# Kernel optimization log

Measured on AMD Instinct MI355X. Metric: run time of the kernel, lower is better.

## Reference

```python
import jax, jax.numpy as jnp
import numpy as np

G, N, E, F, C, H = 2, 20000, 160000, 128, 64, 8
NEG_SLOPE = 0.2


def setup_inputs() -> dict:
    key = jax.random.key(0)
    ks = jax.random.split(key, 16)
    def w(k, shape, fan_in):
        return jax.random.normal(k, shape, jnp.float32) * (1.0 / np.sqrt(fan_in))
    z = lambda *s: jnp.zeros(s, jnp.float32)
    return {
        "x": jax.random.normal(ks[0], (G, N, F), jnp.float32),
        "edge_index": jax.random.randint(ks[1], (G, 2, E), 0, N, jnp.int32),
        "edge_weight": jax.random.uniform(ks[2], (G, E), jnp.float32),
        "Wl1": w(ks[3], (F, H * C), F), "bl1": z(H * C),
        "Wr1": w(ks[4], (F, H * C), F), "br1": z(H * C),
        "We1": w(ks[5], (1, H * C), 1),
        "att1": w(ks[6], (H, C), C),
        "bias1": z(H * C),
        "Wl2": w(ks[7], (H * C, C), H * C), "bl2": z(C),
        "Wr2": w(ks[8], (H * C, C), H * C), "br2": z(C),
        "We2": w(ks[9], (1, C), 1),
        "att2": w(ks[10], (1, C), C),
        "bias2": z(C),
        "Wg": w(ks[11], (C, C), C), "bg": z(C),
        "Wn": w(ks[12], (2 * C, C), 2 * C), "bn": z(C),
        "Wo": w(ks[13], (C, 1), C), "bo": z(1),
    }


def _segment_softmax(logits, seg, n):
    m = jax.ops.segment_max(logits, seg, num_segments=n)
    ex = jnp.exp(logits - m[seg])
    den = jax.ops.segment_sum(ex, seg, num_segments=n)
    return ex / den[seg]


def _gatv2(x, src, dst, eattr, Wl, bl, Wr, br, We, att, bias, heads, concat):
    # Faithful PyG GATv2Conv (share_weights=False, edge_dim=1).
    n = x.shape[0]
    hc = Wl.shape[1]
    c = hc // heads
    xl = (x @ Wl + bl).reshape(n, heads, c)   # lin_l (source / message)
    xr = (x @ Wr + br).reshape(n, heads, c)   # lin_r (target)
    ee = (eattr @ We).reshape(-1, heads, c)   # lin_edge (bias=False)
    s = jax.nn.leaky_relu(xl[src] + xr[dst] + ee, NEG_SLOPE)  # [Etot, H, C]
    logit = jnp.einsum('ehc,hc->eh', s, att)
    alpha = _segment_softmax(logit, dst, n)   # softmax over incoming edges
    out = jax.ops.segment_sum(alpha[..., None] * xl[src], dst, num_segments=n)
    out = out.reshape(n, hc) if concat else out.mean(axis=1)
    return out + bias


def _forward(edge_index, x, edge_weight, Wl1, bl1, Wr1, br1, We1, att1, bias1,
             Wl2, bl2, Wr2, br2, We2, att2, bias2, Wg, bg, Wn, bn, Wo, bo):
    n = x.shape[1]
    def per_graph(xg, eig, ewg):
        src, dst = eig[0], eig[1]
        ea = ewg[:, None]  # edge_weight.unsqueeze(-1), edge_dim=1
        # add_self_loops with fill_value='mean' (mean of edge_attr grouped by dst)
        cnt = jax.ops.segment_sum(jnp.ones_like(ewg), dst, num_segments=n)
        loop = jax.ops.segment_sum(ea, dst, num_segments=n) / jnp.clip(cnt, 1.0)[:, None]
        ar = jnp.arange(n, dtype=src.dtype)
        src2 = jnp.concatenate([src, ar])
        dst2 = jnp.concatenate([dst, ar])
        ea2 = jnp.concatenate([ea, loop], axis=0)
        h = jax.nn.elu(_gatv2(xg, src2, dst2, ea2, Wl1, bl1, Wr1, br1, We1, att1, bias1, H, True))
        h = jax.nn.elu(_gatv2(h, src2, dst2, ea2, Wl2, bl2, Wr2, br2, We2, att2, bias2, 1, False))
        return h
    h = jax.vmap(per_graph)(x, edge_index, edge_weight)      # [G, N, C]
    g_emb = h.max(axis=1)                                    # global_max_pool per graph
    Gv = g_emb.max(axis=0)                                   # max over graphs -> [C]
    Gv = jax.nn.relu(Gv @ Wg + bg)
    Hc = jnp.concatenate([h, jnp.broadcast_to(Gv, h.shape)], axis=-1)  # [G,N,2C]
    h2 = jax.nn.relu(Hc @ Wn + bn)
    return (h2 @ Wo + bo)[..., 0]                            # [G, N] logits


def reference(x, edge_index, edge_weight, Wl1, bl1, Wr1, br1, We1, att1, bias1,
              Wl2, bl2, Wr2, br2, We2, att2, bias2, Wg, bg, Wn, bn, Wo, bo):
    return _forward(edge_index, x, edge_weight, Wl1, bl1, Wr1, br1, We1, att1, bias1,
                    Wl2, bl2, Wr2, br2, We2, att2, bias2, Wg, bg, Wn, bn, Wo, bo)
```

## Files before the change

kernel.cpp:

```cpp
#include <hip/hip_runtime.h>
#include <hip/hip_bf16.h>
#include <cstdint>
#include <cstddef>

#define NEG_SLOPE 0.2f

static constexpr int Gg = 2;
static constexpr int Nn = 20000;
static constexpr int Ee = 160000;
static constexpr int Ff = 128;
static constexpr int Cc = 64;
static constexpr int HC = 512;
static constexpr int GN = Gg * Nn;
static constexpr int GNP = 40064;
static constexpr int DEGMAX = 48;

typedef __attribute__((ext_vector_type(8))) short short8;
typedef __attribute__((ext_vector_type(4))) float floatx4;

__device__ __forceinline__ float bf2f(unsigned short b) {
    return __uint_as_float(((unsigned)b) << 16);
}
__device__ __forceinline__ unsigned short f2bf(float x) {
    unsigned u = __float_as_uint(x);
    unsigned r = 0x7fffu + ((u >> 16) & 1u);
    return (unsigned short)((u + r) >> 16);
}
__device__ __forceinline__ void unpack8(const uint4 p, float* f) {
    f[0] = __uint_as_float(p.x << 16); f[1] = __uint_as_float(p.x & 0xffff0000u);
    f[2] = __uint_as_float(p.y << 16); f[3] = __uint_as_float(p.y & 0xffff0000u);
    f[4] = __uint_as_float(p.z << 16); f[5] = __uint_as_float(p.z & 0xffff0000u);
    f[6] = __uint_as_float(p.w << 16); f[7] = __uint_as_float(p.w & 0xffff0000u);
}
__device__ __forceinline__ void unpack4(const uint2 p, float* f) {
    f[0] = __uint_as_float(p.x << 16); f[1] = __uint_as_float(p.x & 0xffff0000u);
    f[2] = __uint_as_float(p.y << 16); f[3] = __uint_as_float(p.y & 0xffff0000u);
}
__device__ __forceinline__ unsigned encf(float x) {
    unsigned u = __float_as_uint(x);
    return (u & 0x80000000u) ? ~u : (u | 0x80000000u);
}
__device__ __forceinline__ float decf(unsigned e) {
    return __uint_as_float((e & 0x80000000u) ? (e ^ 0x80000000u) : ~e);
}

__global__ void castprep_k(const float* __restrict__ x, unsigned short* __restrict__ xb,
                           const float* __restrict__ Wl1, const float* __restrict__ Wr1,
                           const float* __restrict__ bl1, const float* __restrict__ br1,
                           const float* __restrict__ Wl2, const float* __restrict__ Wr2,
                           const float* __restrict__ bl2, const float* __restrict__ br2,
                           unsigned short* __restrict__ Wt1, unsigned short* __restrict__ Wt2,
                           float* __restrict__ b1cat, float* __restrict__ b2cat,
                           int* __restrict__ cnt, unsigned* __restrict__ gmax) {
    int t = blockIdx.x * 256 + threadIdx.x;
    size_t base = (size_t)t * 4;
    if (base < (size_t)GNP * Ff) {
        ushort4 ov;
        if (base < (size_t)GN * Ff) {
            float4 v = *(const float4*)(x + base);
            ov.x = f2bf(v.x); ov.y = f2bf(v.y); ov.z = f2bf(v.z); ov.w = f2bf(v.w);
        } else {
            ov.x = ov.y = ov.z = ov.w = 0;
        }
        *(ushort4*)(xb + base) = ov;
    }
    if (t < 1024 * 128) {
        int n = t >> 7, k = t & 127;
        float v = (n < 512) ? Wl1[(size_t)k * 512 + n] : Wr1[(size_t)k * 512 + n - 512];
        Wt1[t] = f2bf(v);
    }
    if (t < 128 * 512) {
        int n = t >> 9, k = t & 511;
        float v = (n < 64) ? Wl2[(size_t)k * 64 + n] : Wr2[(size_t)k * 64 + n - 64];
        Wt2[t] = f2bf(v);
    }
    if (t < 1024) b1cat[t] = (t < 512) ? bl1[t] : br1[t - 512];
    if (t < 128)  b2cat[t] = (t < 64) ? bl2[t] : br2[t - 64];
    if (t < GN)   cnt[t] = 0;
    if (t < 1024) gmax[t] = 0u;
}

template <int K, bool EDGES>
__global__ __launch_bounds__(256) void mfma_gemm_k(const unsigned short* __restrict__ A, int lda,
                                                   const unsigned short* __restrict__ Bt,
                                                   const float* __restrict__ bias,
                                                   unsigned short* __restrict__ Cg, int ldc,
                                                   int Mreal,
                                                   const int* __restrict__ ei,
                                                   const float* __restrict__ ew,
                                                   int* __restrict__ cnt,
                                                   int2* __restrict__ sedge) {
    if (EDGES) {
        int bid = blockIdx.y * gridDim.x + blockIdx.x;
        int idx = bid * 256 + threadIdx.x;
        if (idx < Gg * Ee) {
            int g = (idx >= Ee) ? 1 : 0;
            int e = idx - g * Ee;
            int src = ei[(size_t)g * 2 * Ee + e];
            int dst = ei[(size_t)g * 2 * Ee + Ee + e];
            float wv = ew[idx];
            int node = g * Nn + dst;
            int pos = atomicAdd(&cnt[node], 1);
            if (pos < DEGMAX) {
                int2 v; v.x = src; v.y = __float_as_int(wv);
                sedge[(size_t)node * DEGMAX + pos] = v;
            }
        }
    }

    __shared__ unsigned short As[128 * 32];
    __shared__ unsigned short Bs[128 * 32];
    const int t = threadIdx.x;
    const int lane = t & 63;
    const int wid = t >> 6;
    const int wm = wid >> 1, wn = wid & 1;
    const int m0 = blockIdx.x * 128;
    const int n0 = blockIdx.y * 128;

    floatx4 acc[4][4] = {};

    const int jrow = t >> 2;
    const int js = t & 3;
    const int wavebase = (t & 192) * 16;

    for (int k0 = 0; k0 < K; k0 += 32) {
#pragma unroll
        for (int r = 0; r < 2; ++r) {
            int row = jrow + r * 64;
            int c = js ^ ((row >> 1) & 3);
            const unsigned short* gA = A + (size_t)(m0 + row) * lda + k0 + c * 8;
            const unsigned short* gB = Bt + (size_t)(n0 + row) * K + k0 + c * 8;
            __builtin_amdgcn_global_load_lds(
                (const __attribute__((address_space(1))) void*)gA,
                (__attribute__((address_space(3))) void*)((char*)As + r * 4096 + wavebase),
                16, 0, 0);
            __builtin_amdgcn_global_load_lds(
                (const __attribute__((address_space(1))) void*)gB,
                (__attribute__((address_space(3))) void*)((char*)Bs + r * 4096 + wavebase),
                16, 0, 0);
        }
        __syncthreads();

        const int lrow = lane & 15, lc = lane >> 4;
        short8 af[4], bf[4];
#pragma unroll
        for (int i2 = 0; i2 < 4; ++i2) {
            int rA = wm * 64 + i2 * 16 + lrow;
            int sA = lc ^ ((rA >> 1) & 3);
            af[i2] = *(const short8*)((const char*)As + (rA * 4 + sA) * 16);
        }
#pragma unroll
        for (int j2 = 0; j2 < 4; ++j2) {
            int rB = wn * 64 + j2 * 16 + lrow;
            int sB = lc ^ ((rB >> 1) & 3);
            bf[j2] = *(const short8*)((const char*)Bs + (rB * 4 + sB) * 16);
        }
#pragma unroll
        for (int i2 = 0; i2 < 4; ++i2)
#pragma unroll
            for (int j2 = 0; j2 < 4; ++j2)
                acc[i2][j2] = __builtin_amdgcn_mfma_f32_16x16x32_bf16(bf[j2], af[i2], acc[i2][j2], 0, 0, 0);
        __syncthreads();
    }

    const int mrow = m0 + wm * 64 + (lane & 15);
    const int ncol0 = n0 + wn * 64 + ((lane >> 4) << 2);
    float4 bq[4];
#pragma unroll
    for (int j2 = 0; j2 < 4; ++j2) bq[j2] = *(const float4*)(bias + ncol0 + j2 * 16);
#pragma unroll
    for (int i2 = 0; i2 < 4; ++i2) {
        int m = mrow + i2 * 16;
        if (m < Mreal) {
#pragma unroll
            for (int j2 = 0; j2 < 4; ++j2) {
                ushort4 ov;
                ov.x = f2bf(acc[i2][j2][0] + bq[j2].x);
                ov.y = f2bf(acc[i2][j2][1] + bq[j2].y);
                ov.z = f2bf(acc[i2][j2][2] + bq[j2].z);
                ov.w = f2bf(acc[i2][j2][3] + bq[j2].w);
                *(ushort4*)(Cg + (size_t)m * ldc + ncol0 + j2 * 16) = ov;
            }
        }
    }
}

__global__ __launch_bounds__(256) void agg1_k(const unsigned short* xlr,
                                              const int2* __restrict__ sedge,
                                              const int* __restrict__ cnt,
                                              const float* __restrict__ att1, const float* __restrict__ We1,
                                              const float* __restrict__ bias1,
                                              unsigned short* h1, float* __restrict__ loopw) {
    const int lane = threadIdx.x & 63;
    const int node = (blockIdx.x << 2) + (threadIdx.x >> 6);
    if (node >= GN) return;
    const int g = (node >= Nn) ? 1 : 0;

    float attv[8], wev[8];
    {
        float4 a0 = *(const float4*)(att1 + lane * 8);
        float4 a1 = *(const float4*)(att1 + lane * 8 + 4);
        attv[0] = a0.x; attv[1] = a0.y; attv[2] = a0.z; attv[3] = a0.w;
        attv[4] = a1.x; attv[5] = a1.y; attv[6] = a1.z; attv[7] = a1.w;
        float4 w0 = *(const float4*)(We1 + lane * 8);
        float4 w1 = *(const float4*)(We1 + lane * 8 + 4);
        wev[0] = w0.x; wev[1] = w0.y; wev[2] = w0.z; wev[3] = w0.w;
        wev[4] = w1.x; wev[5] = w1.y; wev[6] = w1.z; wev[7] = w1.w;
    }
    float xrv[8];
    unpack8(((const uint4*)(xlr + (size_t)node * 1024 + 512))[lane], xrv);

    const int ec = cnt[node];
    const int2* ep = sedge + (size_t)node * DEGMAX;
    const uint4* rowb = (const uint4*)(xlr + (size_t)g * Nn * 1024) + lane;

    float lsum = 0.f, wsum = 0.f;
    float acc[8] = {};

    uint4 r0, r1; int2 s0v, s1v;
    if (ec > 0) { s0v = ep[0]; r0 = rowb[(size_t)s0v.x * 128]; }
    if (ec > 1) { s1v = ep[1]; r1 = rowb[(size_t)s1v.x * 128]; }
    int e = 0;
    while (e + 1 < ec) {
        uint4 r2, r3; int2 s2v, s3v;
        if (e + 2 < ec) { s2v = ep[e + 2]; r2 = rowb[(size_t)s2v.x * 128]; }
        if (e + 3 < ec) { s3v = ep[e + 3]; r3 = rowb[(size_t)s3v.x * 128]; }
        float xa[8], xb_[8];
        unpack8(r0, xa);
        unpack8(r1, xb_);
        float wa = __int_as_float(s0v.y), wb = __int_as_float(s1v.y);
        wsum += wa + wb;
        float ta = 0.f, tb = 0.f;
#pragma unroll
        for (int j = 0; j < 8; ++j) {
            float sa = xa[j] + fmaf(wa, wev[j], xrv[j]);
            float sb = xb_[j] + fmaf(wb, wev[j], xrv[j]);
            sa = fmaxf(sa, NEG_SLOPE * sa);
            sb = fmaxf(sb, NEG_SLOPE * sb);
            ta = fmaf(sa, attv[j], ta);
            tb = fmaf(sb, attv[j], tb);
        }
        ta += __shfl_xor(ta, 1); tb += __shfl_xor(tb, 1);
        ta += __shfl_xor(ta, 2); tb += __shfl_xor(tb, 2);
        ta += __shfl_xor(ta, 4); tb += __shfl_xor(tb, 4);
        float pa = __expf(ta), pb = __expf(tb);
        lsum += pa + pb;
#pragma unroll
        for (int j = 0; j < 8; ++j) acc[j] = fmaf(pa, xa[j], fmaf(pb, xb_[j], acc[j]));
        r0 = r2; s0v = s2v; r1 = r3; s1v = s3v;
        e += 2;
    }
    if (e < ec) {
        float xa[8];
        unpack8(r0, xa);
        float wa = __int_as_float(s0v.y);
        wsum += wa;
        float ta = 0.f;
#pragma unroll
        for (int j = 0; j < 8; ++j) {
            float sa = xa[j] + fmaf(wa, wev[j], xrv[j]);
            sa = fmaxf(sa, NEG_SLOPE * sa);
            ta = fmaf(sa, attv[j], ta);
        }
        ta += __shfl_xor(ta, 1); ta += __shfl_xor(ta, 2); ta += __shfl_xor(ta, 4);
        float pa = __expf(ta);
        lsum += pa;
#pragma unroll
        for (int j = 0; j < 8; ++j) acc[j] = fmaf(pa, xa[j], acc[j]);
    }

    float lw = wsum / fmaxf((float)ec, 1.f);
    {
        float xv[8];
        unpack8(((const uint4*)(xlr + (size_t)node * 1024))[lane], xv);
        float tp = 0.f;
#pragma unroll
        for (int j = 0; j < 8; ++j) {
            float s = xv[j] + fmaf(lw, wev[j], xrv[j]);
            s = fmaxf(s, NEG_SLOPE * s);
            tp = fmaf(s, attv[j], tp);
        }
        tp += __shfl_xor(tp, 1); tp += __shfl_xor(tp, 2); tp += __shfl_xor(tp, 4);
        float p = __expf(tp);
        lsum += p;
#pragma unroll
        for (int j = 0; j < 8; ++j) acc[j] = fmaf(p, xv[j], acc[j]);
    }

    float inv = 1.f / lsum;
    float4 b0 = *(const float4*)(bias1 + lane * 8);
    float4 b1 = *(const float4*)(bias1 + lane * 8 + 4);
    float bvv[8] = {b0.x, b0.y, b0.z, b0.w, b1.x, b1.y, b1.z, b1.w};
    float ov[8];
#pragma unroll
    for (int j = 0; j < 8; ++j) {
        float o = fmaf(acc[j], inv, bvv[j]);
        ov[j] = o > 0.f ? o : (__expf(o) - 1.f);
    }
    uint4 pk;
    pk.x = (unsigned)f2bf(ov[0]) | ((unsigned)f2bf(ov[1]) << 16);
    pk.y = (unsigned)f2bf(ov[2]) | ((unsigned)f2bf(ov[3]) << 16);
    pk.z = (unsigned)f2bf(ov[4]) | ((unsigned)f2bf(ov[5]) << 16);
    pk.w = (unsigned)f2bf(ov[6]) | ((unsigned)f2bf(ov[7]) << 16);
    ((uint4*)(h1 + (size_t)node * 1024))[lane] = pk;
    if (lane == 0) loopw[node] = lw;
}

__global__ __launch_bounds__(1024) void agg2_k(const unsigned short* __restrict__ xlr2,
                                               const int2* __restrict__ sedge,
                                               const int* __restrict__ cnt,
                                               const float* __restrict__ loopw,
                                               const float* __restrict__ att2, const float* __restrict__ We2,
                                               const float* __restrict__ bias2,
                                               float* __restrict__ hout, unsigned* __restrict__ gmax) {
    const int tid = threadIdx.x;
    const int lane = tid & 63;
    const int cs = lane & 15;
    const int sub = lane >> 4;
    const int node = blockIdx.x * 16 + (tid >> 6);
    const int g = (node >= Nn) ? 1 : 0;

    float4 av = *(const float4*)(att2 + cs * 4);
    float4 wv4 = *(const float4*)(We2 + cs * 4);
    float attv[4] = {av.x, av.y, av.z, av.w};
    float wevv[4] = {wv4.x, wv4.y, wv4.z, wv4.w};
    float xrv[4];
    unpack4(*(const uint2*)(xlr2 + (size_t)node * 128 + 64 + cs * 4), xrv);
    const unsigned short* rowb = xlr2 + (size_t)g * Nn * 128;

    const int ec = cnt[node];
    const int2* ep = sedge + (size_t)node * DEGMAX;
    const int lo = (ec * sub) >> 2;
    const int hi = (ec * (sub + 1)) >> 2;

    float lsum = 0.f, acc[4] = {};

    int e = lo;
    uint2 r0 = {0, 0}, r1 = {0, 0};
    int2 s0v = {0, 0}, s1v = {0, 0};
    if (e < hi)     { s0v = ep[e];     r0 = *(const uint2*)(rowb + (size_t)s0v.x * 128 + cs * 4); }
    if (e + 1 < hi) { s1v = ep[e + 1]; r1 = *(const uint2*)(rowb + (size_t)s1v.x * 128 + cs * 4); }
    while (e + 1 < hi) {
        uint2 r2 = {0, 0}, r3 = {0, 0};
        int2 s2v = {0, 0}, s3v = {0, 0};
        if (e + 2 < hi) { s2v = ep[e + 2]; r2 = *(const uint2*)(rowb + (size_t)s2v.x * 128 + cs * 4); }
        if (e + 3 < hi) { s3v = ep[e + 3]; r3 = *(const uint2*)(rowb + (size_t)s3v.x * 128 + cs * 4); }
        float xa[4], xb_[4];
        unpack4(r0, xa);
        unpack4(r1, xb_);
        float wa = __int_as_float(s0v.y), wb = __int_as_float(s1v.y);
        float ta = 0.f, tb = 0.f;
#pragma unroll
        for (int j = 0; j < 4; ++j) {
            float sa = xa[j] + fmaf(wa, wevv[j], xrv[j]);
            float sb = xb_[j] + fmaf(wb, wevv[j], xrv[j]);
            sa = fmaxf(sa, NEG_SLOPE * sa);
            sb = fmaxf(sb, NEG_SLOPE * sb);
            ta = fmaf(sa, attv[j], ta);
            tb = fmaf(sb, attv[j], tb);
        }
        ta += __shfl_xor(ta, 1); tb += __shfl_xor(tb, 1);
        ta += __shfl_xor(ta, 2); tb += __shfl_xor(tb, 2);
        ta += __shfl_xor(ta, 4); tb += __shfl_xor(tb, 4);
        ta += __shfl_xor(ta, 8); tb += __shfl_xor(tb, 8);
        float pa = __expf(ta), pb = __expf(tb);
        lsum += pa + pb;
#pragma unroll
        for (int j = 0; j < 4; ++j) acc[j] = fmaf(pa, xa[j], fmaf(pb, xb_[j], acc[j]));
        r0 = r2; s0v = s2v; r1 = r3; s1v = s3v;
        e += 2;
    }
    if (e < hi) {
        float xa[4];
        unpack4(r0, xa);
        float wa = __int_as_float(s0v.y);
        float ta = 0.f;
#pragma unroll
        for (int j = 0; j < 4; ++j) {
            float sa = xa[j] + fmaf(wa, wevv[j], xrv[j]);
            sa = fmaxf(sa, NEG_SLOPE * sa);
            ta = fmaf(sa, attv[j], ta);
        }
        ta += __shfl_xor(ta, 1); ta += __shfl_xor(ta, 2);
        ta += __shfl_xor(ta, 4); ta += __shfl_xor(ta, 8);
        float pa = __expf(ta);
        lsum += pa;
#pragma unroll
        for (int j = 0; j < 4; ++j) acc[j] = fmaf(pa, xa[j], acc[j]);
    }

    lsum += __shfl_xor(lsum, 16); lsum += __shfl_xor(lsum, 32);
#pragma unroll
    for (int j = 0; j < 4; ++j) {
        acc[j] += __shfl_xor(acc[j], 16);
        acc[j] += __shfl_xor(acc[j], 32);
    }

    {
        float lw = loopw[node];
        float xv[4];
        unpack4(*(const uint2*)(xlr2 + (size_t)node * 128 + cs * 4), xv);
        float tp = 0.f;
#pragma unroll
        for (int j = 0; j < 4; ++j) {
            float s = xv[j] + fmaf(lw, wevv[j], xrv[j]);
            s = fmaxf(s, NEG_SLOPE * s);
            tp = fmaf(s, attv[j], tp);
        }
        tp += __shfl_xor(tp, 1); tp += __shfl_xor(tp, 2);
        tp += __shfl_xor(tp, 4); tp += __shfl_xor(tp, 8);
        float p = __expf(tp);
        lsum += p;
#pragma unroll
        for (int j = 0; j < 4; ++j) acc[j] = fmaf(p, xv[j], acc[j]);
    }

    float inv = 1.f / lsum;
    float4 bv = *(const float4*)(bias2 + cs * 4);
    float bvv[4] = {bv.x, bv.y, bv.z, bv.w};
    float ov[4];
#pragma unroll
    for (int j = 0; j < 4; ++j) {
        float o = fmaf(acc[j], inv, bvv[j]);
        ov[j] = o > 0.f ? o : (__expf(o) - 1.f);
    }
    if (sub == 0) {
        float4 o4;
        o4.x = ov[0]; o4.y = ov[1]; o4.z = ov[2]; o4.w = ov[3];
        *(float4*)(hout + (size_t)node * Cc + cs * 4) = o4;
    }

    __shared__ unsigned bm[64];
    if (tid < 64) bm[tid] = 0u;
    __syncthreads();
    if (sub == 0) {
#pragma unroll
        for (int j = 0; j < 4; ++j) atomicMax(&bm[cs * 4 + j], encf(ov[j]));
    }
    __syncthreads();
    if (tid < 64) atomicMax(&gmax[tid * 16], bm[tid]);
}

__global__ __launch_bounds__(256) void final_k(const float* __restrict__ h,
                                               const unsigned* __restrict__ gmax,
                                               const float* __restrict__ Wg, const float* __restrict__ bg,
                                               const float* __restrict__ Wn, const float* __restrict__ bn,
                                               const float* __restrict__ Wo, const float* __restrict__ bo,
                                               float* __restrict__ out) {
    __shared__ float wns[64 * 64];
    __shared__ float g0s[64], g1s[64], cvs[64];
    const int tid = threadIdx.x;
    for (int k = tid; k < 64 * 64; k += 256) wns[k] = Wn[k];
    if (tid < 64) g0s[tid] = decf(gmax[tid * 16]);
    __syncthreads();
    if (tid < 64) {
        float a = bg[tid];
        for (int c = 0; c < 64; ++c) a += g0s[c] * Wg[c * 64 + tid];
        g1s[tid] = fmaxf(a, 0.f);
    }
    __syncthreads();
    if (tid < 64) {
        float b = bn[tid];
        for (int c = 0; c < 64; ++c) b += g1s[c] * Wn[(64 + c) * 64 + tid];
        cvs[tid] = b;
    }
    __syncthreads();

    const int lane = tid & 63;
    const int cs = lane & 15;
    const int sub = lane >> 4;
    const int node = blockIdx.x * 16 + (tid >> 6) * 4 + sub;

    float4 h4 = *(const float4*)(h + (size_t)node * Cc + cs * 4);
    float hv[4] = {h4.x, h4.y, h4.z, h4.w};
    float inner[4] = {cvs[cs * 4 + 0], cvs[cs * 4 + 1], cvs[cs * 4 + 2], cvs[cs * 4 + 3]};
#pragma unroll
    for (int c = 0; c < 64; ++c) {
        float hc = __shfl(hv[c & 3], sub * 16 + (c >> 2));
        float4 wv = *(const float4*)&wns[c * 64 + cs * 4];
        inner[0] = fmaf(hc, wv.x, inner[0]);
        inner[1] = fmaf(hc, wv.y, inner[1]);
        inner[2] = fmaf(hc, wv.z, inner[2]);
        inner[3] = fmaf(hc, wv.w, inner[3]);
    }
    float4 wo4 = *(const float4*)(Wo + cs * 4);
    float woa[4] = {wo4.x, wo4.y, wo4.z, wo4.w};
    float t = 0.f;
#pragma unroll
    for (int j = 0; j < 4; ++j) {
        float v = fmaxf(inner[j], 0.f);
        t = fmaf(v, woa[j], t);
    }
    t += __shfl_xor(t, 1); t += __shfl_xor(t, 2);
    t += __shfl_xor(t, 4); t += __shfl_xor(t, 8);
    if (cs == 0) out[node] = t + bo[0];
}

extern "C" void kernel_launch(void* const* d_in, const int* in_sizes, int n_in,
                              void* d_out, int out_size, void* d_ws, size_t ws_size,
                              hipStream_t stream) {
    const float* x     = (const float*)d_in[0];
    const int*   ei    = (const int*)d_in[1];
    const float* ew    = (const float*)d_in[2];
    const float* Wl1   = (const float*)d_in[3];
    const float* bl1v  = (const float*)d_in[4];
    const float* Wr1   = (const float*)d_in[5];
    const float* br1v  = (const float*)d_in[6];
    const float* We1   = (const float*)d_in[7];
    const float* att1  = (const float*)d_in[8];
    const float* bias1 = (const float*)d_in[9];
    const float* Wl2   = (const float*)d_in[10];
    const float* bl2v  = (const float*)d_in[11];
    const float* Wr2   = (const float*)d_in[12];
    const float* br2v  = (const float*)d_in[13];
    const float* We2   = (const float*)d_in[14];
    const float* att2  = (const float*)d_in[15];
    const float* bias2 = (const float*)d_in[16];
    const float* Wg    = (const float*)d_in[17];
    const float* bgv   = (const float*)d_in[18];
    const float* Wn    = (const float*)d_in[19];
    const float* bnv   = (const float*)d_in[20];
    const float* Wo    = (const float*)d_in[21];
    const float* bov   = (const float*)d_in[22];
    float* out = (float*)d_out;

    char* w = (char*)d_ws;
    size_t o = 0;
    auto take = [&](size_t b) -> char* {
        char* p = w + o;
        o += (b + 255) & ~(size_t)255;
        return p;
    };
    unsigned short* xlr1 = (unsigned short*)take((size_t)GNP * 1024 * 2);
    unsigned short* xb   = (unsigned short*)take((size_t)GNP * Ff * 2);
    unsigned short* xlr2 = (unsigned short*)take((size_t)GNP * 128 * 2);
    unsigned short* Wt1  = (unsigned short*)take(1024 * 128 * 2);
    unsigned short* Wt2  = (unsigned short*)take(128 * 512 * 2);
    float* b1cat = (float*)take(1024 * 4);
    float* b2cat = (float*)take(128 * 4);
    int*    cnt   = (int*)take((size_t)GN * 4);
    float*  loopw = (float*)take((size_t)GN * 4);
    int2*   sedge = (int2*)take((size_t)GN * DEGMAX * 8);
    unsigned* gmax = (unsigned*)take(1024 * 4);
    unsigned short* h1 = xlr1 + 512;
    float* hbuf = (float*)xb;

    castprep_k<<<((GNP * Ff / 4) + 255) / 256, 256, 0, stream>>>(
        x, xb, Wl1, Wr1, bl1v, br1v, Wl2, Wr2, bl2v, br2v, Wt1, Wt2, b1cat, b2cat, cnt, gmax);

    mfma_gemm_k<Ff, true><<<dim3(GNP / 128, 8), 256, 0, stream>>>(
        xb, Ff, Wt1, b1cat, xlr1, 1024, GN, ei, ew, cnt, sedge);

    agg1_k<<<GN / 4, 256, 0, stream>>>(xlr1, sedge, cnt, att1, We1, bias1, h1, loopw);

    mfma_gemm_k<HC, false><<<dim3(GNP / 128, 1), 256, 0, stream>>>(
        h1, 1024, Wt2, b2cat, xlr2, 128, GN, nullptr, nullptr, nullptr, nullptr);

    agg2_k<<<GN / 16, 1024, 0, stream>>>(xlr2, sedge, cnt, loopw, att2, We2, bias2, hbuf, gmax);

    final_k<<<GN / 16, 256, 0, stream>>>(hbuf, gmax, Wg, bgv, Wn, bnv, Wo, bov, out);

    (void)in_sizes; (void)n_in; (void)out_size; (void)ws_size;
}
```

Before: 330.8 us.

## Split layer-1 source features into per-head planes and aggregate one head per wave

The first GEMM now writes the source projection (xl) as eight head-major planes of 64 channels and the target projection into a separate buffer. The layer-1 aggregation runs one wavefront per (head, node), and its eight lane-octets each process a different incoming edge, followed by a cross-octet shuffle reduction. The aim is to shrink the gathered working set per pass so each head's plane is more cache-resident, and to get more edge-level parallelism. In exchange there are eight times as many waves, each re-reading the edge list and repeating the per-node setup, and there is extra shuffle-reduction work.

```diff
diff --git a/kernel.cpp b/kernel.cpp
--- a/kernel.cpp
+++ b/kernel.cpp
@@ -80,12 +80,12 @@
     if (t < 1024) gmax[t] = 0u;
 }
 
-template <int K, bool EDGES>
+template <int K, bool EDGES, bool SPLIT>
 __global__ __launch_bounds__(256) void mfma_gemm_k(const unsigned short* __restrict__ A, int lda,
                                                    const unsigned short* __restrict__ Bt,
                                                    const float* __restrict__ bias,
                                                    unsigned short* __restrict__ Cg, int ldc,
-                                                   int Mreal,
+                                                   int Mreal, unsigned short* __restrict__ Cxr,
                                                    const int* __restrict__ ei,
                                                    const float* __restrict__ ew,
                                                    int* __restrict__ cnt,
@@ -174,105 +174,115 @@
         if (m < Mreal) {
 #pragma unroll
             for (int j2 = 0; j2 < 4; ++j2) {
+                int ncol = ncol0 + j2 * 16;
                 ushort4 ov;
                 ov.x = f2bf(acc[i2][j2][0] + bq[j2].x);
                 ov.y = f2bf(acc[i2][j2][1] + bq[j2].y);
                 ov.z = f2bf(acc[i2][j2][2] + bq[j2].z);
                 ov.w = f2bf(acc[i2][j2][3] + bq[j2].w);
-                *(ushort4*)(Cg + (size_t)m * ldc + ncol0 + j2 * 16) = ov;
+                unsigned short* dst;
+                if (SPLIT) {
+                    if (ncol < 512)
+                        dst = Cg + (((size_t)(ncol >> 6) * GNP) + m) * 64 + (ncol & 63);
+                    else
+                        dst = Cxr + (size_t)m * 512 + (ncol - 512);
+                } else {
+                    dst = Cg + (size_t)m * ldc + ncol;
+                }
+                *(ushort4*)dst = ov;
             }
         }
     }
 }
 
-__global__ __launch_bounds__(256) void agg1_k(const unsigned short* xlr,
+__global__ __launch_bounds__(256) void agg1_k(const unsigned short* __restrict__ xlh,
+                                              const unsigned short* xr,
                                               const int2* __restrict__ sedge,
                                               const int* __restrict__ cnt,
                                               const float* __restrict__ att1, const float* __restrict__ We1,
                                               const float* __restrict__ bias1,
                                               unsigned short* h1, float* __restrict__ loopw) {
     const int lane = threadIdx.x & 63;
-    const int node = (blockIdx.x << 2) + (threadIdx.x >> 6);
-    if (node >= GN) return;
+    const int oct = lane >> 3;
+    const int ci  = lane & 7;
+    const int W = blockIdx.x * 4 + (threadIdx.x >> 6);
+    const int head = W / GN;
+    const int node = W - head * GN;
     const int g = (node >= Nn) ? 1 : 0;
-
-    float attv[8], wev[8];
+    const int cb = head * 64 + ci * 8;
+
+    float attv[8], wev[8], xrv[8], bvv[8];
     {
-        float4 a0 = *(const float4*)(att1 + lane * 8);
-        float4 a1 = *(const float4*)(att1 + lane * 8 + 4);
+        float4 a0 = *(const float4*)(att1 + cb);
+        float4 a1 = *(const float4*)(att1 + cb + 4);
         attv[0] = a0.x; attv[1] = a0.y; attv[2] = a0.z; attv[3] = a0.w;
         attv[4] = a1.x; attv[5] = a1.y; attv[6] = a1.z; attv[7] = a1.w;
-        float4 w0 = *(const float4*)(We1 + lane * 8);
-        float4 w1 = *(const float4*)(We1 + lane * 8 + 4);
+        float4 w0 = *(const float4*)(We1 + cb);
+        float4 w1 = *(const float4*)(We1 + cb + 4);
         wev[0] = w0.x; wev[1] = w0.y; wev[2] = w0.z; wev[3] = w0.w;
         wev[4] = w1.x; wev[5] = w1.y; wev[6] = w1.z; wev[7] = w1.w;
-    }
-    float xrv[8];
-    unpack8(((const uint4*)(xlr + (size_t)node * 1024 + 512))[lane], xrv);
+        float4 b0 = *(const float4*)(bias1 + cb);
+        float4 b1 = *(const float4*)(bias1 + cb + 4);
+        bvv[0] = b0.x; bvv[1] = b0.y; bvv[2] = b0.z; bvv[3] = b0.w;
+        bvv[4] = b1.x; bvv[5] = b1.y; bvv[6] = b1.z; bvv[7] = b1.w;
+        unpack8(*(const uint4*)(xr + (size_t)node * 512 + cb), xrv);
+    }
 
     const int ec = cnt[node];
     const int2* ep = sedge + (size_t)node * DEGMAX;
-    const uint4* rowb = (const uint4*)(xlr + (size_t)g * Nn * 1024) + lane;
+    const unsigned short* plane = xlh + ((size_t)head * GNP + (size_t)g * Nn) * 64;
 
     float lsum = 0.f, wsum = 0.f;
     float acc[8] = {};
 
-    uint4 r0, r1; int2 s0v, s1v;
-    if (ec > 0) { s0v = ep[0]; r0 = rowb[(size_t)s0v.x * 128]; }
-    if (ec > 1) { s1v = ep[1]; r1 = rowb[(size_t)s1v.x * 128]; }
-    int e = 0;
-    while (e + 1 < ec) {
-        uint4 r2, r3; int2 s2v, s3v;
-        if (e + 2 < ec) { s2v = ep[e + 2]; r2 = rowb[(size_t)s2v.x * 128]; }
-        if (e + 3 < ec) { s3v = ep[e + 3]; r3 = rowb[(size_t)s3v.x * 128]; }
-        float xa[8], xb_[8];
-        unpack8(r0, xa);
-        unpack8(r1, xb_);
-        float wa = __int_as_float(s0v.y), wb = __int_as_float(s1v.y);
-        wsum += wa + wb;
-        float ta = 0.f, tb = 0.f;
+    int eb = 0;
+    int2 sv; uint4 r;
+    if (ec > 0) {
+        int e = min(eb + oct, ec - 1);
+        sv = ep[e];
+        r = *(const uint4*)(plane + (size_t)sv.x * 64 + ci * 8);
+    }
+    while (eb < ec) {
+        int2 svn; uint4 rn;
+        int ebn = eb + 8;
+        if (ebn < ec) {
+            int e2 = min(ebn + oct, ec - 1);
+            svn = ep[e2];
+            rn = *(const uint4*)(plane + (size_t)svn.x * 64 + ci * 8);
+        }
+        float xa[8];
+        unpack8(r, xa);
+        float wa = __int_as_float(sv.y);
+        float tp = 0.f;
 #pragma unroll
         for (int j = 0; j < 8; ++j) {
-            float sa = xa[j] + fmaf(wa, wev[j], xrv[j]);
-            float sb = xb_[j] + fmaf(wb, wev[j], xrv[j]);
-            sa = fmaxf(sa, NEG_SLOPE * sa);
-            sb = fmaxf(sb, NEG_SLOPE * sb);
-            ta = fmaf(sa, attv[j], ta);
-            tb = fmaf(sb, attv[j], tb);
-        }
-        ta += __shfl_xor(ta, 1); tb += __shfl_xor(tb, 1);
-        ta += __shfl_xor(ta, 2); tb += __shfl_xor(tb, 2);
-        ta += __shfl_xor(ta, 4); tb += __shfl_xor(tb, 4);
-        float pa = __expf(ta), pb = __expf(tb);
-        lsum += pa + pb;
-#pragma unroll
-        for (int j = 0; j < 8; ++j) acc[j] = fmaf(pa, xa[j], fmaf(pb, xb_[j], acc[j]));
-        r0 = r2; s0v = s2v; r1 = r3; s1v = s3v;
-        e += 2;
-    }
-    if (e < ec) {
-        float xa[8];
-        unpack8(r0, xa);
-        float wa = __int_as_float(s0v.y);
-        wsum += wa;
-        float ta = 0.f;
-#pragma unroll
-        for (int j = 0; j < 8; ++j) {
-            float sa = xa[j] + fmaf(wa, wev[j], xrv[j]);
-            sa = fmaxf(sa, NEG_SLOPE * sa);
-            ta = fmaf(sa, attv[j], ta);
-        }
-        ta += __shfl_xor(ta, 1); ta += __shfl_xor(ta, 2); ta += __shfl_xor(ta, 4);
-        float pa = __expf(ta);
-        lsum += pa;
-#pragma unroll
-        for (int j = 0; j < 8; ++j) acc[j] = fmaf(pa, xa[j], acc[j]);
+            float s = xa[j] + fmaf(wa, wev[j], xrv[j]);
+            s = fmaxf(s, NEG_SLOPE * s);
+            tp = fmaf(s, attv[j], tp);
+        }
+        tp += __shfl_xor(tp, 1); tp += __shfl_xor(tp, 2); tp += __shfl_xor(tp, 4);
+        bool valid = (eb + oct) < ec;
+        float p = valid ? __expf(tp) : 0.f;
+        lsum += p;
+        if (valid) wsum += wa;
+#pragma unroll
+        for (int j = 0; j < 8; ++j) acc[j] = fmaf(p, xa[j], acc[j]);
+        sv = svn; r = rn; eb = ebn;
+    }
+
+    lsum += __shfl_xor(lsum, 8); lsum += __shfl_xor(lsum, 16); lsum += __shfl_xor(lsum, 32);
+    wsum += __shfl_xor(wsum, 8); wsum += __shfl_xor(wsum, 16); wsum += __shfl_xor(wsum, 32);
+#pragma unroll
+    for (int j = 0; j < 8; ++j) {
+        acc[j] += __shfl_xor(acc[j], 8);
+        acc[j] += __shfl_xor(acc[j], 16);
+        acc[j] += __shfl_xor(acc[j], 32);
     }
 
     float lw = wsum / fmaxf((float)ec, 1.f);
     {
         float xv[8];
-        unpack8(((const uint4*)(xlr + (size_t)node * 1024))[lane], xv);
+        unpack8(*(const uint4*)(xlh + ((size_t)head * GNP + node) * 64 + ci * 8), xv);
         float tp = 0.f;
 #pragma unroll
         for (int j = 0; j < 8; ++j) {
@@ -288,22 +298,21 @@
     }
 
     float inv = 1.f / lsum;
-    float4 b0 = *(const float4*)(bias1 + lane * 8);
-    float4 b1 = *(const float4*)(bias1 + lane * 8 + 4);
-    float bvv[8] = {b0.x, b0.y, b0.z, b0.w, b1.x, b1.y, b1.z, b1.w};
     float ov[8];
 #pragma unroll
     for (int j = 0; j < 8; ++j) {
         float o = fmaf(acc[j], inv, bvv[j]);
         ov[j] = o > 0.f ? o : (__expf(o) - 1.f);
     }
-    uint4 pk;
-    pk.x = (unsigned)f2bf(ov[0]) | ((unsigned)f2bf(ov[1]) << 16);
-    pk.y = (unsigned)f2bf(ov[2]) | ((unsigned)f2bf(ov[3]) << 16);
-    pk.z = (unsigned)f2bf(ov[4]) | ((unsigned)f2bf(ov[5]) << 16);
-    pk.w = (unsigned)f2bf(ov[6]) | ((unsigned)f2bf(ov[7]) << 16);
-    ((uint4*)(h1 + (size_t)node * 1024))[lane] = pk;
-    if (lane == 0) loopw[node] = lw;
+    if (oct == 0) {
+        uint4 pk;
+        pk.x = (unsigned)f2bf(ov[0]) | ((unsigned)f2bf(ov[1]) << 16);
+        pk.y = (unsigned)f2bf(ov[2]) | ((unsigned)f2bf(ov[3]) << 16);
+        pk.z = (unsigned)f2bf(ov[4]) | ((unsigned)f2bf(ov[5]) << 16);
+        pk.w = (unsigned)f2bf(ov[6]) | ((unsigned)f2bf(ov[7]) << 16);
+        *(uint4*)(h1 + (size_t)node * 512 + cb) = pk;
+    }
+    if (head == 0 && lane == 0) loopw[node] = lw;
 }
 
 __global__ __launch_bounds__(1024) void agg2_k(const unsigned short* __restrict__ xlr2,
@@ -531,7 +540,8 @@
         o += (b + 255) & ~(size_t)255;
         return p;
     };
-    unsigned short* xlr1 = (unsigned short*)take((size_t)GNP * 1024 * 2);
+    unsigned short* xlh  = (unsigned short*)take((size_t)8 * GNP * 64 * 2);
+    unsigned short* xr   = (unsigned short*)take((size_t)GNP * 512 * 2);
     unsigned short* xb   = (unsigned short*)take((size_t)GNP * Ff * 2);
     unsigned short* xlr2 = (unsigned short*)take((size_t)GNP * 128 * 2);
     unsigned short* Wt1  = (unsigned short*)take(1024 * 128 * 2);
@@ -542,19 +552,19 @@
     float*  loopw = (float*)take((size_t)GN * 4);
     int2*   sedge = (int2*)take((size_t)GN * DEGMAX * 8);
     unsigned* gmax = (unsigned*)take(1024 * 4);
-    unsigned short* h1 = xlr1 + 512;
+    unsigned short* h1 = xr;
     float* hbuf = (float*)xb;
 
     castprep_k<<<((GNP * Ff / 4) + 255) / 256, 256, 0, stream>>>(
         x, xb, Wl1, Wr1, bl1v, br1v, Wl2, Wr2, bl2v, br2v, Wt1, Wt2, b1cat, b2cat, cnt, gmax);
 
-    mfma_gemm_k<Ff, true><<<dim3(GNP / 128, 8), 256, 0, stream>>>(
-        xb, Ff, Wt1, b1cat, xlr1, 1024, GN, ei, ew, cnt, sedge);
-
-    agg1_k<<<GN / 4, 256, 0, stream>>>(xlr1, sedge, cnt, att1, We1, bias1, h1, loopw);
-
-    mfma_gemm_k<HC, false><<<dim3(GNP / 128, 1), 256, 0, stream>>>(
-        h1, 1024, Wt2, b2cat, xlr2, 128, GN, nullptr, nullptr, nullptr, nullptr);
+    mfma_gemm_k<Ff, true, true><<<dim3(GNP / 128, 8), 256, 0, stream>>>(
+        xb, Ff, Wt1, b1cat, xlh, 0, GN, xr, ei, ew, cnt, sedge);
+
+    agg1_k<<<(8 * GN) / 4, 256, 0, stream>>>(xlh, xr, sedge, cnt, att1, We1, bias1, h1, loopw);
+
+    mfma_gemm_k<HC, false, false><<<dim3(GNP / 128, 1), 256, 0, stream>>>(
+        h1, 512, Wt2, b2cat, xlr2, 128, GN, nullptr, nullptr, nullptr, nullptr, nullptr);
 
     agg2_k<<<GN / 16, 1024, 0, stream>>>(xlr2, sedge, cnt, loopw, att2, We2, bias2, hbuf, gmax);
 
```

New measurement: 460.1 us. 1.39x slower.
